# Performance work log

Measured on AMD Instinct MI355X. Metric: run time of the kernel, lower is better.

## Reference

```python
import jax, jax.numpy as jnp
import numpy as np
from jax import lax

# ---- dims / config (see init_kwargs) ----
M_IMG, N_PCD, C = 1008, 1024, 256     # coarse img nodes (24*32+12*16+6*8), coarse pcd nodes, feat dim
NI_F, NP_F = 76800, 30000             # fine img pixels (240*320), fine pcd points
KI, KP = 64, 64                       # knn patch sizes
NUM_CORR, TOPK = 256, 3               # coarse matching params
COARSE_THR, FINE_THR = 0.0, 0.0       # similarity thresholds (lowered for random data)


def _norm(x):
    return x / (jnp.linalg.norm(x, axis=-1, keepdims=True) + 1e-8)


def setup_inputs() -> dict:
    key = jax.random.key(0)
    ks = jax.random.split(key, 7)
    return {
        "img_feats_c": _norm(jax.random.normal(ks[0], (M_IMG, C), jnp.float32)),
        "pcd_feats_c": _norm(jax.random.normal(ks[1], (N_PCD, C), jnp.float32)),
        "img_feats_f": _norm(jax.random.normal(ks[2], (NI_F, C), jnp.float32)),
        "pcd_feats_f": _norm(jax.random.normal(ks[3], (NP_F, C), jnp.float32)),
        "img_node_masks": jnp.ones((M_IMG,), bool),
        "pcd_node_masks": jnp.ones((N_PCD,), bool),
        "img_node_knn_indices": jax.random.randint(ks[4], (M_IMG, KI), 0, NI_F),
        "pcd_node_knn_indices": jax.random.randint(ks[5], (N_PCD, KP), 0, NP_F),
        "pcd_node_knn_masks": jax.random.uniform(ks[6], (N_PCD, KP)) > 0.1,
    }


def _coarse_match(img_feats_c, pcd_feats_c, img_masks, pcd_masks):
    # SuperPointMatchingMutualTopk: cosine sim + mutual top-k + global top NUM_CORR
    sim = img_feats_c @ pcd_feats_c.T                              # [M, N] (feats normalized)
    valid = img_masks[:, None] & pcd_masks[None, :]
    sim_m = jnp.where(valid, sim, -jnp.inf)
    row_kth = lax.top_k(sim_m, TOPK)[0][:, -1:]                    # kth-largest per row [M,1]
    col_kth = lax.top_k(sim_m.T, TOPK)[0][:, -1:].T                # kth-largest per col [1,N]
    mutual = (sim_m >= row_kth) & (sim_m >= col_kth) & (sim_m > COARSE_THR)
    flat = jnp.where(mutual, sim_m, -jnp.inf).ravel()
    vals, flat_idx = lax.top_k(flat, NUM_CORR)                     # fixed-size selection
    img_idx = flat_idx // N_PCD
    pcd_idx = flat_idx % N_PCD
    corr_valid = jnp.isfinite(vals)
    return img_idx, pcd_idx, corr_valid


def reference(img_feats_c, pcd_feats_c, img_feats_f, pcd_feats_f,
              img_node_masks, pcd_node_masks,
              img_node_knn_indices, pcd_node_knn_indices, pcd_node_knn_masks):
    # ---- coarse matching ----
    img_idx, pcd_idx, corr_valid = _coarse_match(
        img_feats_c, pcd_feats_c, img_node_masks, pcd_node_masks)

    # ---- fine matching: knn gather + pairwise cosine + mutual top-1 ----
    pcd_padded = jnp.concatenate([pcd_feats_f, jnp.zeros_like(pcd_feats_f[:1])], axis=0)
    img_knn_idx = img_node_knn_indices[img_idx]                    # [Ci, KI]
    pcd_knn_idx = pcd_node_knn_indices[pcd_idx]                    # [Ci, KP]
    pcd_knn_msk = pcd_node_knn_masks[pcd_idx]                      # [Ci, KP]
    img_knn_feats = img_feats_f[img_knn_idx]                       # [Ci, KI, C]
    pcd_knn_feats = pcd_padded[pcd_knn_idx]                        # [Ci, KP, C]

    sim = jnp.einsum('bic,bjc->bij', img_knn_feats, pcd_knn_feats) # [Ci, KI, KP]
    m3 = corr_valid[:, None, None] & pcd_knn_msk[:, None, :]
    sim = jnp.where(m3, sim, -jnp.inf)

    row_best = jnp.argmax(sim, axis=2)                             # [Ci, KI]
    row_val = jnp.max(sim, axis=2)
    col_best = jnp.argmax(sim, axis=1)                             # [Ci, KP]
    back = jnp.take_along_axis(col_best, row_best, axis=1)         # [Ci, KI]
    sel = (back == jnp.arange(KI)[None, :]) & jnp.isfinite(row_val) & (row_val > FINE_THR)

    img_corr = img_knn_idx.reshape(-1)                             # [Ci*KI]
    pcd_corr = jnp.take_along_axis(pcd_knn_idx, row_best, axis=1).reshape(-1)
    sel = sel.reshape(-1)
    # sentinel for unselected pairs -> sorts last
    img_corr = jnp.where(sel, img_corr, NI_F)
    pcd_corr = jnp.where(sel, pcd_corr, NP_F)

    # ---- dedup (torch.unique on img*Npf+pcd) via lexsort + first-occurrence mask ----
    order = jnp.lexsort((pcd_corr, img_corr))
    ic, pc = img_corr[order], pcd_corr[order]
    first = jnp.concatenate([jnp.array([True]),
                             (ic[1:] != ic[:-1]) | (pc[1:] != pc[:-1])])
    valid = first & (ic < NI_F)

    ic_s = jnp.clip(ic, 0, NI_F - 1)
    pc_s = jnp.clip(pc, 0, NP_F - 1)
    corr_scores = jnp.sum(img_feats_f[ic_s] * pcd_feats_f[pc_s], axis=1)
    corr_scores = corr_scores * valid.astype(corr_scores.dtype)    # masked scores [Ci*KI]
    return corr_scores
```

## Files before the change

kernel.cpp:

```cpp
#include <hip/hip_runtime.h>

#define M_IMG 1008
#define N_PCD 1024
#define CDIM  256
#define NI_F  76800
#define NP_F  30000
#define KI    64
#define KP    64
#define NUM_CORR 256
#define NPAIR (NUM_CORR * KI)
#define KEY_MOD 30001u
#define NCAND (M_IMG * 3)
#define NEG_INF (-__builtin_inff())

__device__ __forceinline__ bool mask_val(const void* p, int i, int is_u8) {
    return is_u8 ? (((const unsigned char*)p)[i] != 0)
                 : (((const int*)p)[i] != 0);
}

__device__ __forceinline__ void top3_insert(float v, float& t0, float& t1, float& t2) {
    if (v > t0) { t2 = t1; t1 = t0; t0 = v; }
    else if (v > t1) { t2 = t1; t1 = v; }
    else if (v > t2) { t2 = v; }
}

__device__ __forceinline__ void top3_merge(float a0, float a1, float a2,
                                           float b0, float b1, float b2,
                                           float& x0, float& x1, float& x2) {
    if (a0 >= b0) {
        x0 = a0;
        if (a1 >= b0) { x1 = a1; x2 = (a2 >= b0) ? a2 : b0; }
        else          { x1 = b0; x2 = (a1 >= b1) ? a1 : b1; }
    } else {
        x0 = b0;
        if (b1 >= a0) { x1 = b1; x2 = (b2 >= a0) ? b2 : a0; }
        else          { x1 = a0; x2 = (b1 >= a1) ? b1 : a1; }
    }
}

__device__ __forceinline__ void t3i_insert(float v, int i,
                                           float& v0, int& i0,
                                           float& v1, int& i1,
                                           float& v2, int& i2) {
    if (v > v0) { v2 = v1; i2 = i1; v1 = v0; i1 = i0; v0 = v; i0 = i; }
    else if (v > v1) { v2 = v1; i2 = i1; v1 = v; i1 = i; }
    else if (v > v2) { v2 = v; i2 = i; }
}

__global__ void coarse_topk_kernel(const float* __restrict__ A,
                                   const float* __restrict__ B,
                                   const void* __restrict__ maskA,
                                   const void* __restrict__ maskB,
                                   const unsigned int* __restrict__ mskw,
                                   float* __restrict__ rowp,
                                   int* __restrict__ rowpi,
                                   float* __restrict__ colp,
                                   float* __restrict__ out0,
                                   unsigned int* __restrict__ cnt,
                                   int* __restrict__ nk) {
    __shared__ __align__(16) float s_a[32][36];
    __shared__ __align__(16) float s_b[32][68];
    __shared__ float srv[32][16][3];
    __shared__ int   sri[32][16][3];
    __shared__ float scv[64][16][2];
    const int m0 = blockIdx.y * 32, n0 = blockIdx.x * 64;
    const int tid = threadIdx.x;
    const int tx = tid & 15, ty = tid >> 4;
    const int c_lane = tid & 31;
    const int r_base = tid >> 5;
    const int bx = blockIdx.x;

    const int bid = blockIdx.y * 16 + blockIdx.x;
    if (tid < 32) out0[bid * 32 + tid] = 0.f;
    if (tid >= 32 && tid < 64) cnt[bid * 32 + (tid - 32)] = 0u;
    if (bid == 0 && tid == 64) *nk = 0;

    const bool hit = (mskw[tid] & 0xFFFFFF00u) != 0u;

    const float* pa[4];
    const float* pb[8];
#pragma unroll
    for (int k = 0; k < 4; k++) {
        int m = m0 + r_base + 8 * k;
        pa[k] = A + (size_t)(m < M_IMG ? m : 0) * CDIM + c_lane;
    }
#pragma unroll
    for (int k = 0; k < 8; k++)
        pb[k] = B + (size_t)(n0 + r_base + 8 * k) * CDIM + c_lane;

    float ra[4], rb[8];
#pragma unroll
    for (int k = 0; k < 4; k++) ra[k] = pa[k][0];
#pragma unroll
    for (int k = 0; k < 8; k++) rb[k] = pb[k][0];
#pragma unroll
    for (int k = 0; k < 4; k++) s_a[c_lane][r_base + 8 * k] = ra[k];
#pragma unroll
    for (int k = 0; k < 8; k++) s_b[c_lane][r_base + 8 * k] = rb[k];
    __syncthreads();

    float acc[2][4];
#pragma unroll
    for (int r = 0; r < 2; r++)
#pragma unroll
        for (int j = 0; j < 4; j++) acc[r][j] = 0.f;

    for (int cit = 0; cit < 8; cit++) {
        if (cit < 7) {
            const int cc = (cit + 1) * 32;
#pragma unroll
            for (int k = 0; k < 4; k++) ra[k] = pa[k][cc];
#pragma unroll
            for (int k = 0; k < 8; k++) rb[k] = pb[k][cc];
        }
#pragma unroll 8
        for (int c = 0; c < 32; c++) {
            float2 av = *(const float2*)&s_a[c][ty * 2];
            float4 bv = *(const float4*)&s_b[c][tx * 4];
            float ar[2] = {av.x, av.y};
            float br[4] = {bv.x, bv.y, bv.z, bv.w};
#pragma unroll
            for (int r = 0; r < 2; r++)
#pragma unroll
                for (int j = 0; j < 4; j++) acc[r][j] += ar[r] * br[j];
        }
        __syncthreads();
        if (cit < 7) {
#pragma unroll
            for (int k = 0; k < 4; k++) s_a[c_lane][r_base + 8 * k] = ra[k];
#pragma unroll
            for (int k = 0; k < 8; k++) s_b[c_lane][r_base + 8 * k] = rb[k];
            __syncthreads();
        }
    }

    const int is_u8 = __syncthreads_or(hit ? 1 : 0);

    float mv[2][4];
#pragma unroll
    for (int r = 0; r < 2; r++) {
        int m = m0 + ty * 2 + r;
        bool ma = (m < M_IMG) ? mask_val(maskA, m, is_u8) : false;
#pragma unroll
        for (int j = 0; j < 4; j++) {
            int n = n0 + tx * 4 + j;
            bool ok = ma && mask_val(maskB, n, is_u8);
            mv[r][j] = ok ? acc[r][j] : NEG_INF;
        }
    }

#pragma unroll
    for (int r = 0; r < 2; r++) {
        float v0 = NEG_INF, v1 = NEG_INF, v2 = NEG_INF;
        int i0 = 0, i1 = 0, i2 = 0;
#pragma unroll
        for (int j = 0; j < 4; j++)
            t3i_insert(mv[r][j], n0 + tx * 4 + j, v0, i0, v1, i1, v2, i2);
        const int row = ty * 2 + r;
        srv[row][tx][0] = v0; srv[row][tx][1] = v1; srv[row][tx][2] = v2;
        sri[row][tx][0] = i0; sri[row][tx][1] = i1; sri[row][tx][2] = i2;
    }
#pragma unroll
    for (int j = 0; j < 4; j++) {
        float a = mv[0][j], b = mv[1][j];
        scv[tx * 4 + j][ty][0] = fmaxf(a, b);
        scv[tx * 4 + j][ty][1] = fminf(a, b);
    }
    __syncthreads();

    if (tid < 32) {
        const int m = m0 + tid;
        if (m < M_IMG) {
            float v0 = srv[tid][0][0], v1 = srv[tid][0][1], v2 = srv[tid][0][2];
            int   i0 = sri[tid][0][0], i1 = sri[tid][0][1], i2 = sri[tid][0][2];
            for (int t = 1; t < 16; t++)
#pragma unroll
                for (int k = 0; k < 3; k++)
                    t3i_insert(srv[tid][t][k], sri[tid][t][k],
                               v0, i0, v1, i1, v2, i2);
            const int pb0 = bx * 3;
            rowp [(pb0 + 0) * M_IMG + m] = v0; rowpi[(pb0 + 0) * M_IMG + m] = i0;
            rowp [(pb0 + 1) * M_IMG + m] = v1; rowpi[(pb0 + 1) * M_IMG + m] = i1;
            rowp [(pb0 + 2) * M_IMG + m] = v2; rowpi[(pb0 + 2) * M_IMG + m] = i2;
        }
    } else if (tid >= 64 && tid < 128) {
        const int c = tid - 64;
        float t0 = scv[c][0][0], t1 = scv[c][0][1], t2 = NEG_INF;
        for (int t = 1; t < 16; t++) {
            top3_insert(scv[c][t][0], t0, t1, t2);
            top3_insert(scv[c][t][1], t0, t1, t2);
        }
        const int n = n0 + c;
        colp[(0 * 32 + blockIdx.y) * N_PCD + n] = t0;
        colp[(1 * 32 + blockIdx.y) * N_PCD + n] = t1;
        colp[(2 * 32 + blockIdx.y) * N_PCD + n] = t2;
    }
}

__global__ void merge_kernel(const float* __restrict__ rowp,
                             const int* __restrict__ rowpi,
                             const float* __restrict__ colp,
                             float* __restrict__ rowv3,
                             int* __restrict__ rowi3,
                             float* __restrict__ col_kth) {
    __shared__ float sv[4][64][3];
    __shared__ int   si[4][64][3];
    const int tid = threadIdx.x;
    const int lane = tid & 63, qq = tid >> 6;
    if (blockIdx.x < 16) {
        const int m = blockIdx.x * 64 + lane;
        float v0 = NEG_INF, v1 = NEG_INF, v2 = NEG_INF;
        int i0 = 0, i1 = 0, i2 = 0;
        if (m < M_IMG) {
#pragma unroll
            for (int k = 0; k < 4; k++) {
                const int sx = qq * 4 + k;
#pragma unroll
                for (int s = 0; s < 3; s++)
                    t3i_insert(rowp[(sx * 3 + s) * M_IMG + m],
                               rowpi[(sx * 3 + s) * M_IMG + m],
                               v0, i0, v1, i1, v2, i2);
            }
        }
        sv[qq][lane][0] = v0; sv[qq][lane][1] = v1; sv[qq][lane][2] = v2;
        si[qq][lane][0] = i0; si[qq][lane][1] = i1; si[qq][lane][2] = i2;
        __syncthreads();
        if (qq == 0 && m < M_IMG) {
            for (int q = 1; q < 4; q++)
#pragma unroll
                for (int s = 0; s < 3; s++)
                    t3i_insert(sv[q][lane][s], si[q][lane][s],
                               v0, i0, v1, i1, v2, i2);
            rowv3[m * 3 + 0] = v0; rowi3[m * 3 + 0] = i0;
            rowv3[m * 3 + 1] = v1; rowi3[m * 3 + 1] = i1;
            rowv3[m * 3 + 2] = v2; rowi3[m * 3 + 2] = i2;
        }
    } else {
        const int n = (blockIdx.x - 16) * 64 + lane;
        float t0 = NEG_INF, t1 = NEG_INF, t2 = NEG_INF;
#pragma unroll
        for (int k = 0; k < 8; k++) {
            const int ch = qq * 8 + k;
            float b0 = colp[(0 * 32 + ch) * N_PCD + n];
            float b1 = colp[(1 * 32 + ch) * N_PCD + n];
            float b2 = colp[(2 * 32 + ch) * N_PCD + n];
            float x0, x1, x2;
            top3_merge(t0, t1, t2, b0, b1, b2, x0, x1, x2);
            t0 = x0; t1 = x1; t2 = x2;
        }
        sv[qq][lane][0] = t0; sv[qq][lane][1] = t1; sv[qq][lane][2] = t2;
        __syncthreads();
        if (qq == 0) {
            for (int q = 1; q < 4; q++) {
                float x0, x1, x2;
                top3_merge(t0, t1, t2,
                           sv[q][lane][0], sv[q][lane][1], sv[q][lane][2],
                           x0, x1, x2);
                t0 = x0; t1 = x1; t2 = x2;
            }
            col_kth[n] = t2;
        }
    }
}

__global__ __launch_bounds__(1024)
void select_kernel(const float* __restrict__ rowv3,
                   const int* __restrict__ rowi3,
                   const float* __restrict__ col_kth,
                   int* __restrict__ sel_idx,
                   int* __restrict__ selK) {
    __shared__ float s_colk[N_PCD];
    __shared__ __align__(16) unsigned long long s_key[NCAND];
    __shared__ int s_part[1024];
    __shared__ int s_wsum[16];
    const int tid = threadIdx.x;
    const int lane = tid & 63, w = tid >> 6;

    s_colk[tid] = col_kth[tid];
    __syncthreads();

    unsigned long long k0 = 0, k1 = 0, k2 = 0;
    int f0 = 0, f1 = 0, f2 = 0;
    if (tid < M_IMG) {
#pragma unroll
        for (int s = 0; s < 3; s++) {
            float v = rowv3[tid * 3 + s];
            int n = rowi3[tid * 3 + s];
            if (v > 0.f && v >= s_colk[n]) {
                unsigned int u = __float_as_uint(v);
                unsigned int mono = (u & 0x80000000u) ? ~u : (u | 0x80000000u);
                unsigned long long key =
                    ((unsigned long long)(~mono) << 32)
                    | (unsigned int)(tid * N_PCD + n);
                if (s == 0) { k0 = key; f0 = 1; }
                else if (s == 1) { k1 = key; f1 = 1; }
                else { k2 = key; f2 = 1; }
            }
        }
    }
    const int c = f0 + f1 + f2;

    int v = c;
#pragma unroll
    for (int d = 1; d < 64; d <<= 1) {
        int o = __shfl_up(v, d);
        if (lane >= d) v += o;
    }
    if (lane == 63) s_wsum[w] = v;
    __syncthreads();
    if (w == 0) {
        int x = (lane < 16) ? s_wsum[lane] : 0;
#pragma unroll
        for (int d = 1; d < 16; d <<= 1) {
            int o = __shfl_up(x, d);
            if (lane >= d) x += o;
        }
        if (lane < 16) s_wsum[lane] = x;
    }
    __syncthreads();
    const int K = s_wsum[15];
    int pos = v - c + (w > 0 ? s_wsum[w - 1] : 0);

    if (f0) s_key[pos++] = k0;
    if (f1) s_key[pos++] = k1;
    if (f2) s_key[pos++] = k2;
    __syncthreads();

    if (blockIdx.x == 0 && tid == 0) *selK = (K < NUM_CORR) ? K : NUM_CORR;

    const int ii = tid & 255, q = tid >> 8;
    const int i = blockIdx.x * 256 + ii;
    const unsigned long long my = (i < K) ? s_key[i] : 0xFFFFFFFFFFFFFFFFull;
    int less = 0;
    for (int j = q; j < K; j += 4)
        less += (s_key[j] < my);
    s_part[tid] = less;
    __syncthreads();
    if (q == 0 && i < K) {
        int rank = s_part[ii] + s_part[ii + 256] + s_part[ii + 512] + s_part[ii + 768];
        if (rank < NUM_CORR)
            sel_idx[rank] = (int)(s_key[i] & 0xFFFFFFFFull);
    }
}

__global__ void fine_kernel(const float* __restrict__ img_f,
                            const float* __restrict__ pcd_f,
                            const int* __restrict__ img_knn,
                            const int* __restrict__ pcd_knn,
                            const void* __restrict__ pcd_msk,
                            const unsigned int* __restrict__ mskw,
                            const int* __restrict__ sel_idx,
                            const int* __restrict__ selK_ptr,
                            int* __restrict__ nk,
                            unsigned int* __restrict__ ckeys,
                            float* __restrict__ cscore) {
    const int ci = blockIdx.x, tid = threadIdx.x;
    if (ci >= *selK_ptr) return;
    __shared__ int s_ik[KI], s_pk[KP];
    __shared__ unsigned char s_mk[KP];
    __shared__ __align__(16) float s_a[32][68];
    __shared__ __align__(16) float s_b[32][68];
    __shared__ float s_sim[64][65];
    __shared__ int s_rb[64], s_cb[64];
    __shared__ float s_rv[64];

    const bool hit = (mskw[tid & 255] & 0xFFFFFF00u) != 0u;
    int flat = sel_idx[ci];
    int gi = flat >> 10, pi = flat & 1023;
    if (tid < 64) {
        s_ik[tid] = img_knn[gi * KI + tid];
        s_pk[tid] = pcd_knn[pi * KP + tid];
    }
    const int is_u8 = __syncthreads_or(hit ? 1 : 0);
    if (tid < 64)
        s_mk[tid] = mask_val(pcd_msk, pi * KP + tid, is_u8) ? 1 : 0;

    const int tx = tid & 15, tyy = tid >> 4;
    const int c_lane = tid & 31;
    const int r_base = tid >> 5;

    const float* pa[4];
    const float* pb[4];
#pragma unroll
    for (int k = 0; k < 4; k++) {
        pa[k] = img_f + (size_t)s_ik[r_base + 16 * k] * CDIM + c_lane;
        pb[k] = pcd_f + (size_t)s_pk[r_base + 16 * k] * CDIM + c_lane;
    }

    float ra[4], rb[4];
#pragma unroll
    for (int k = 0; k < 4; k++) { ra[k] = pa[k][0]; rb[k] = pb[k][0]; }
#pragma unroll
    for (int k = 0; k < 4; k++) {
        s_a[c_lane][r_base + 16 * k] = ra[k];
        s_b[c_lane][r_base + 16 * k] = rb[k];
    }
    __syncthreads();

    float acc[2][4];
#pragma unroll
    for (int r = 0; r < 2; r++)
#pragma unroll
        for (int j = 0; j < 4; j++) acc[r][j] = 0.f;

    for (int cit = 0; cit < 8; cit++) {
        if (cit < 7) {
            const int cc = (cit + 1) * 32;
#pragma unroll
            for (int k = 0; k < 4; k++) { ra[k] = pa[k][cc]; rb[k] = pb[k][cc]; }
        }
#pragma unroll 8
        for (int c = 0; c < 32; c++) {
            float2 av = *(const float2*)&s_a[c][tyy * 2];
            float4 bv = *(const float4*)&s_b[c][tx * 4];
            float ar[2] = {av.x, av.y};
            float br[4] = {bv.x, bv.y, bv.z, bv.w};
#pragma unroll
            for (int r = 0; r < 2; r++)
#pragma unroll
                for (int j = 0; j < 4; j++) acc[r][j] += ar[r] * br[j];
        }
        __syncthreads();
        if (cit < 7) {
#pragma unroll
            for (int k = 0; k < 4; k++) {
                s_a[c_lane][r_base + 16 * k] = ra[k];
                s_b[c_lane][r_base + 16 * k] = rb[k];
            }
            __syncthreads();
        }
    }
#pragma unroll
    for (int r = 0; r < 2; r++) {
        int row = tyy * 2 + r;
#pragma unroll
        for (int j = 0; j < 4; j++) {
            int kp = tx * 4 + j;
            s_sim[row][kp] = (s_mk[kp] != 0) ? acc[r][j] : NEG_INF;
        }
    }
    __syncthreads();

    if (tid < 64) {
        float best = NEG_INF; int bi = 0;
        for (int kp = 0; kp < 64; kp++) {
            float v = s_sim[tid][kp];
            if (v > best) { best = v; bi = kp; }
        }
        s_rb[tid] = bi; s_rv[tid] = best;
    } else if (tid < 128) {
        int kp = tid - 64;
        float best = NEG_INF; int bi = 0;
        for (int k2 = 0; k2 < 64; k2++) {
            float v = s_sim[k2][kp];
            if (v > best) { best = v; bi = k2; }
        }
        s_cb[kp] = bi;
    }
    __syncthreads();

    if (tid < 64) {
        int rb2 = s_rb[tid];
        float rv = s_rv[tid];
        if ((s_cb[rb2] == tid) && (rv > 0.f)) {
            int ik = s_ik[tid];
            int pk = s_pk[rb2];
            unsigned int key = (unsigned int)ik * KEY_MOD + (unsigned int)pk;
            const float4* a = (const float4*)(img_f + (size_t)ik * CDIM);
            const float4* b = (const float4*)(pcd_f + (size_t)pk * CDIM);
            float s = 0.f;
#pragma unroll 8
            for (int c = 0; c < CDIM / 4; c++) {
                float4 x = a[c], y = b[c];
                s += x.x * y.x + x.y * y.y + x.z * y.z + x.w * y.w;
            }
            int pos = atomicAdd(nk, 1);
            ckeys[pos] = key;
            cscore[pos] = s;
        }
    }
}

__global__ void rank_count_kernel(const unsigned int* __restrict__ ckeys,
                                  const int* __restrict__ nk,
                                  unsigned int* __restrict__ cnt) {
    const int K = *nk;
    const int bi = blockIdx.x, bj = blockIdx.y;
    if (bi * 256 >= K || bj * 256 >= K) return;
    __shared__ unsigned int s_k[256];
    const int tid = threadIdx.x;
    const int i = bi * 256 + tid;
    const unsigned int myKey = (i < K) ? ckeys[i] : 0xFFFFFFFFu;
    const int j = bj * 256 + tid;
    s_k[tid] = (j < K) ? ckeys[j] : 0xFFFFFFFFu;
    __syncthreads();

    unsigned int less = 0, eqb = 0;
    if (bj < bi) {
#pragma unroll 8
        for (int t = 0; t < 256; t++) {
            unsigned int k = s_k[t];
            less += (k < myKey);
            eqb += (k == myKey);
        }
    } else if (bj == bi) {
#pragma unroll 8
        for (int t = 0; t < 256; t++) {
            unsigned int k = s_k[t];
            less += (k < myKey);
            eqb += (k == myKey) & (t < tid);
        }
    } else {
#pragma unroll 8
        for (int t = 0; t < 256; t++) {
            unsigned int k = s_k[t];
            less += (k < myKey);
        }
    }
    unsigned int v = (less << 16) | eqb;
    if (i < K && v) atomicAdd(&cnt[i], v);
}

__global__ void rank_out_kernel(const unsigned int* __restrict__ cnt,
                                const float* __restrict__ cscore,
                                const int* __restrict__ nk,
                                float* __restrict__ out) {
    const int K = *nk;
    const int i = blockIdx.x * 256 + threadIdx.x;
    if (i >= K) return;
    const unsigned int v = cnt[i];
    if ((v & 0xFFFFu) == 0)
        out[v >> 16] = cscore[i];
}

extern "C" void kernel_launch(void* const* d_in, const int* in_sizes, int n_in,
                              void* d_out, int out_size, void* d_ws, size_t ws_size,
                              hipStream_t stream) {
    const float* img_c = (const float*)d_in[0];
    const float* pcd_c = (const float*)d_in[1];
    const float* img_f = (const float*)d_in[2];
    const float* pcd_f = (const float*)d_in[3];
    const void* img_mask = d_in[4];
    const void* pcd_mask = d_in[5];
    const int* img_knn = (const int*)d_in[6];
    const int* pcd_knn = (const int*)d_in[7];
    const void* pcd_knn_msk = d_in[8];
    float* out = (float*)d_out;

    char* w = (char*)d_ws;
    size_t off = 0;
    float* rowp = (float*)(w + off);           off += 16 * 3 * M_IMG * 4;
    int* rowpi = (int*)(w + off);              off += 16 * 3 * M_IMG * 4;
    float* colp = (float*)(w + off);           off += 3 * 32 * N_PCD * 4;
    float* rowv3 = (float*)(w + off);          off += M_IMG * 3 * 4;
    int* rowi3 = (int*)(w + off);              off += M_IMG * 3 * 4;
    float* col_kth = (float*)(w + off);        off += N_PCD * 4;
    int* sel_idx = (int*)(w + off);            off += NUM_CORR * 4;
    int* selK = (int*)(w + off);               off += 4;
    int* nk = (int*)(w + off);                 off += 4;
    unsigned int* ckeys = (unsigned int*)(w + off); off += NPAIR * 4;
    float* cscore = (float*)(w + off);         off += NPAIR * 4;
    unsigned int* cnt = (unsigned int*)(w + off);   off += NPAIR * 4;

    const unsigned int* mskw = (const unsigned int*)pcd_knn_msk;

    coarse_topk_kernel<<<dim3(16, 32), 256, 0, stream>>>(
        img_c, pcd_c, img_mask, pcd_mask, mskw, rowp, rowpi, colp, out, cnt, nk);
    merge_kernel<<<32, 256, 0, stream>>>(rowp, rowpi, colp, rowv3, rowi3, col_kth);
    select_kernel<<<12, 1024, 0, stream>>>(rowv3, rowi3, col_kth, sel_idx, selK);
    fine_kernel<<<NUM_CORR, 512, 0, stream>>>(img_f, pcd_f, img_knn, pcd_knn,
                                              pcd_knn_msk, mskw, sel_idx, selK,
                                              nk, ckeys, cscore);
    rank_count_kernel<<<dim3(64, 64), 256, 0, stream>>>(ckeys, nk, cnt);
    rank_out_kernel<<<64, 256, 0, stream>>>(cnt, cscore, nk, out);
}
```

Measured before the change: 261.8 us.

## Double-buffer coarse GEMM tiles, shuffle-reduce top-3, fuse rank kernels

The coarse similarity kernel now double-buffers its shared-memory tiles, which removes one barrier per K-chunk. Its row and column top-3 reductions now use wavefront shuffles plus a small cross-wave shared merge, replacing the single-thread serial scans over shared arrays. The two-pass rank count (2D grid with atomics) and the separate output kernel are merged into one kernel where each block loops over all key tiles. This drops the cnt buffer, its zeroing, the atomics and one launch, at the cost of fewer parallel blocks for the rank step.

```diff
diff --git a/kernel.cpp b/kernel.cpp
--- a/kernel.cpp
+++ b/kernel.cpp
@@ -56,24 +56,22 @@
                                    int* __restrict__ rowpi,
                                    float* __restrict__ colp,
                                    float* __restrict__ out0,
-                                   unsigned int* __restrict__ cnt,
                                    int* __restrict__ nk) {
-    __shared__ __align__(16) float s_a[32][36];
-    __shared__ __align__(16) float s_b[32][68];
-    __shared__ float srv[32][16][3];
-    __shared__ int   sri[32][16][3];
-    __shared__ float scv[64][16][2];
+    __shared__ __align__(16) float s_a[2][32][36];
+    __shared__ __align__(16) float s_b[2][32][68];
+    __shared__ float scw[4][3][68];
     const int m0 = blockIdx.y * 32, n0 = blockIdx.x * 64;
     const int tid = threadIdx.x;
     const int tx = tid & 15, ty = tid >> 4;
     const int c_lane = tid & 31;
     const int r_base = tid >> 5;
     const int bx = blockIdx.x;
+    const int wv = tid >> 6;
+    const int g = (tid >> 4) & 3;
 
     const int bid = blockIdx.y * 16 + blockIdx.x;
     if (tid < 32) out0[bid * 32 + tid] = 0.f;
-    if (tid >= 32 && tid < 64) cnt[bid * 32 + (tid - 32)] = 0u;
-    if (bid == 0 && tid == 64) *nk = 0;
+    if (bid == 0 && tid == 32) *nk = 0;
 
     const bool hit = (mskw[tid] & 0xFFFFFF00u) != 0u;
 
@@ -94,9 +92,9 @@
 #pragma unroll
     for (int k = 0; k < 8; k++) rb[k] = pb[k][0];
 #pragma unroll
-    for (int k = 0; k < 4; k++) s_a[c_lane][r_base + 8 * k] = ra[k];
-#pragma unroll
-    for (int k = 0; k < 8; k++) s_b[c_lane][r_base + 8 * k] = rb[k];
+    for (int k = 0; k < 4; k++) s_a[0][c_lane][r_base + 8 * k] = ra[k];
+#pragma unroll
+    for (int k = 0; k < 8; k++) s_b[0][c_lane][r_base + 8 * k] = rb[k];
     __syncthreads();
 
     float acc[2][4];
@@ -105,6 +103,7 @@
 #pragma unroll
         for (int j = 0; j < 4; j++) acc[r][j] = 0.f;
 
+    int cur = 0;
     for (int cit = 0; cit < 8; cit++) {
         if (cit < 7) {
             const int cc = (cit + 1) * 32;
@@ -115,8 +114,8 @@
         }
 #pragma unroll 8
         for (int c = 0; c < 32; c++) {
-            float2 av = *(const float2*)&s_a[c][ty * 2];
-            float4 bv = *(const float4*)&s_b[c][tx * 4];
+            float2 av = *(const float2*)&s_a[cur][c][ty * 2];
+            float4 bv = *(const float4*)&s_b[cur][c][tx * 4];
             float ar[2] = {av.x, av.y};
             float br[4] = {bv.x, bv.y, bv.z, bv.w};
 #pragma unroll
@@ -124,13 +123,13 @@
 #pragma unroll
                 for (int j = 0; j < 4; j++) acc[r][j] += ar[r] * br[j];
         }
-        __syncthreads();
         if (cit < 7) {
 #pragma unroll
-            for (int k = 0; k < 4; k++) s_a[c_lane][r_base + 8 * k] = ra[k];
-#pragma unroll
-            for (int k = 0; k < 8; k++) s_b[c_lane][r_base + 8 * k] = rb[k];
+            for (int k = 0; k < 4; k++) s_a[cur ^ 1][c_lane][r_base + 8 * k] = ra[k];
+#pragma unroll
+            for (int k = 0; k < 8; k++) s_b[cur ^ 1][c_lane][r_base + 8 * k] = rb[k];
             __syncthreads();
+            cur ^= 1;
         }
     }
 
@@ -156,41 +155,61 @@
 #pragma unroll
         for (int j = 0; j < 4; j++)
             t3i_insert(mv[r][j], n0 + tx * 4 + j, v0, i0, v1, i1, v2, i2);
-        const int row = ty * 2 + r;
-        srv[row][tx][0] = v0; srv[row][tx][1] = v1; srv[row][tx][2] = v2;
-        sri[row][tx][0] = i0; sri[row][tx][1] = i1; sri[row][tx][2] = i2;
-    }
+#pragma unroll
+        for (int ms = 1; ms <= 8; ms <<= 1) {
+            float o0 = __shfl_xor(v0, ms), o1 = __shfl_xor(v1, ms), o2 = __shfl_xor(v2, ms);
+            int   a0 = __shfl_xor(i0, ms), a1 = __shfl_xor(i1, ms), a2 = __shfl_xor(i2, ms);
+            t3i_insert(o0, a0, v0, i0, v1, i1, v2, i2);
+            t3i_insert(o1, a1, v0, i0, v1, i1, v2, i2);
+            t3i_insert(o2, a2, v0, i0, v1, i1, v2, i2);
+        }
+        if (tx == 0) {
+            const int m = m0 + ty * 2 + r;
+            if (m < M_IMG) {
+                const int pb0 = bx * 3;
+                rowp [(pb0 + 0) * M_IMG + m] = v0; rowpi[(pb0 + 0) * M_IMG + m] = i0;
+                rowp [(pb0 + 1) * M_IMG + m] = v1; rowpi[(pb0 + 1) * M_IMG + m] = i1;
+                rowp [(pb0 + 2) * M_IMG + m] = v2; rowpi[(pb0 + 2) * M_IMG + m] = i2;
+            }
+        }
+    }
+
+    float c0[4], c1[4], c2[4];
 #pragma unroll
     for (int j = 0; j < 4; j++) {
         float a = mv[0][j], b = mv[1][j];
-        scv[tx * 4 + j][ty][0] = fmaxf(a, b);
-        scv[tx * 4 + j][ty][1] = fminf(a, b);
-    }
-    __syncthreads();
-
-    if (tid < 32) {
-        const int m = m0 + tid;
-        if (m < M_IMG) {
-            float v0 = srv[tid][0][0], v1 = srv[tid][0][1], v2 = srv[tid][0][2];
-            int   i0 = sri[tid][0][0], i1 = sri[tid][0][1], i2 = sri[tid][0][2];
-            for (int t = 1; t < 16; t++)
-#pragma unroll
-                for (int k = 0; k < 3; k++)
-                    t3i_insert(srv[tid][t][k], sri[tid][t][k],
-                               v0, i0, v1, i1, v2, i2);
-            const int pb0 = bx * 3;
-            rowp [(pb0 + 0) * M_IMG + m] = v0; rowpi[(pb0 + 0) * M_IMG + m] = i0;
-            rowp [(pb0 + 1) * M_IMG + m] = v1; rowpi[(pb0 + 1) * M_IMG + m] = i1;
-            rowp [(pb0 + 2) * M_IMG + m] = v2; rowpi[(pb0 + 2) * M_IMG + m] = i2;
-        }
-    } else if (tid >= 64 && tid < 128) {
-        const int c = tid - 64;
-        float t0 = scv[c][0][0], t1 = scv[c][0][1], t2 = NEG_INF;
-        for (int t = 1; t < 16; t++) {
-            top3_insert(scv[c][t][0], t0, t1, t2);
-            top3_insert(scv[c][t][1], t0, t1, t2);
-        }
-        const int n = n0 + c;
+        c0[j] = fmaxf(a, b); c1[j] = fminf(a, b); c2[j] = NEG_INF;
+    }
+#pragma unroll
+    for (int ms = 16; ms <= 32; ms <<= 1) {
+#pragma unroll
+        for (int j = 0; j < 4; j++) {
+            float o0 = __shfl_xor(c0[j], ms), o1 = __shfl_xor(c1[j], ms), o2 = __shfl_xor(c2[j], ms);
+            top3_insert(o0, c0[j], c1[j], c2[j]);
+            top3_insert(o1, c0[j], c1[j], c2[j]);
+            top3_insert(o2, c0[j], c1[j], c2[j]);
+        }
+    }
+    if (g == 0) {
+#pragma unroll
+        for (int j = 0; j < 4; j++) {
+            scw[wv][0][tx * 4 + j] = c0[j];
+            scw[wv][1][tx * 4 + j] = c1[j];
+            scw[wv][2][tx * 4 + j] = c2[j];
+        }
+    }
+    __syncthreads();
+    if (tid < 64) {
+        float t0 = scw[0][0][tid], t1 = scw[0][1][tid], t2 = scw[0][2][tid];
+#pragma unroll
+        for (int w2 = 1; w2 < 4; w2++) {
+            float x0, x1, x2;
+            top3_merge(t0, t1, t2,
+                       scw[w2][0][tid], scw[w2][1][tid], scw[w2][2][tid],
+                       x0, x1, x2);
+            t0 = x0; t1 = x1; t2 = x2;
+        }
+        const int n = n0 + tid;
         colp[(0 * 32 + blockIdx.y) * N_PCD + n] = t0;
         colp[(1 * 32 + blockIdx.y) * N_PCD + n] = t1;
         colp[(2 * 32 + blockIdx.y) * N_PCD + n] = t2;
@@ -481,56 +500,33 @@
     }
 }
 
-__global__ void rank_count_kernel(const unsigned int* __restrict__ ckeys,
-                                  const int* __restrict__ nk,
-                                  unsigned int* __restrict__ cnt) {
+__global__ void rank_kernel(const unsigned int* __restrict__ ckeys,
+                            const int* __restrict__ nk,
+                            const float* __restrict__ cscore,
+                            float* __restrict__ out) {
+    __shared__ unsigned int s_k[256];
     const int K = *nk;
-    const int bi = blockIdx.x, bj = blockIdx.y;
-    if (bi * 256 >= K || bj * 256 >= K) return;
-    __shared__ unsigned int s_k[256];
-    const int tid = threadIdx.x;
+    const int bi = blockIdx.x, tid = threadIdx.x;
+    if (bi * 256 >= K) return;
     const int i = bi * 256 + tid;
     const unsigned int myKey = (i < K) ? ckeys[i] : 0xFFFFFFFFu;
-    const int j = bj * 256 + tid;
-    s_k[tid] = (j < K) ? ckeys[j] : 0xFFFFFFFFu;
-    __syncthreads();
-
-    unsigned int less = 0, eqb = 0;
-    if (bj < bi) {
+    int less = 0, eqb = 0;
+    const int nb = (K + 255) >> 8;
+    for (int bj = 0; bj < nb; bj++) {
+        const int j = bj * 256 + tid;
+        s_k[tid] = (j < K) ? ckeys[j] : 0xFFFFFFFFu;
+        __syncthreads();
+        const int jbase = bj * 256;
 #pragma unroll 8
         for (int t = 0; t < 256; t++) {
             unsigned int k = s_k[t];
             less += (k < myKey);
-            eqb += (k == myKey);
-        }
-    } else if (bj == bi) {
-#pragma unroll 8
-        for (int t = 0; t < 256; t++) {
-            unsigned int k = s_k[t];
-            less += (k < myKey);
-            eqb += (k == myKey) & (t < tid);
-        }
-    } else {
-#pragma unroll 8
-        for (int t = 0; t < 256; t++) {
-            unsigned int k = s_k[t];
-            less += (k < myKey);
-        }
-    }
-    unsigned int v = (less << 16) | eqb;
-    if (i < K && v) atomicAdd(&cnt[i], v);
-}
-
-__global__ void rank_out_kernel(const unsigned int* __restrict__ cnt,
-                                const float* __restrict__ cscore,
-                                const int* __restrict__ nk,
-                                float* __restrict__ out) {
-    const int K = *nk;
-    const int i = blockIdx.x * 256 + threadIdx.x;
-    if (i >= K) return;
-    const unsigned int v = cnt[i];
-    if ((v & 0xFFFFu) == 0)
-        out[v >> 16] = cscore[i];
+            eqb  += (k == myKey) & ((jbase + t) < i);
+        }
+        __syncthreads();
+    }
+    if (i < K && eqb == 0)
+        out[less] = cscore[i];
 }
 
 extern "C" void kernel_launch(void* const* d_in, const int* in_sizes, int n_in,
@@ -560,17 +556,15 @@
     int* nk = (int*)(w + off);                 off += 4;
     unsigned int* ckeys = (unsigned int*)(w + off); off += NPAIR * 4;
     float* cscore = (float*)(w + off);         off += NPAIR * 4;
-    unsigned int* cnt = (unsigned int*)(w + off);   off += NPAIR * 4;
 
     const unsigned int* mskw = (const unsigned int*)pcd_knn_msk;
 
     coarse_topk_kernel<<<dim3(16, 32), 256, 0, stream>>>(
-        img_c, pcd_c, img_mask, pcd_mask, mskw, rowp, rowpi, colp, out, cnt, nk);
+        img_c, pcd_c, img_mask, pcd_mask, mskw, rowp, rowpi, colp, out, nk);
     merge_kernel<<<32, 256, 0, stream>>>(rowp, rowpi, colp, rowv3, rowi3, col_kth);
     select_kernel<<<12, 1024, 0, stream>>>(rowv3, rowi3, col_kth, sel_idx, selK);
     fine_kernel<<<NUM_CORR, 512, 0, stream>>>(img_f, pcd_f, img_knn, pcd_knn,
                                               pcd_knn_msk, mskw, sel_idx, selK,
                                               nk, ckeys, cscore);
-    rank_count_kernel<<<dim3(64, 64), 256, 0, stream>>>(ckeys, nk, cnt);
-    rank_out_kernel<<<64, 256, 0, stream>>>(cnt, cscore, nk, out);
-}
+    rank_kernel<<<64, 256, 0, stream>>>(ckeys, nk, cscore, out);
+}
```

New measurement: 438.0 us. 1.67x slower.
